# Kernel optimization log

Hardware: AMD Instinct MI355X
Metric: run time of the kernel (lower is better)

Reference implementation:

```python
import jax, jax.numpy as jnp
import numpy as np

N, D, B, C, T, TOD = 8192, 32, 2, 8, 12, 288
PARAM_SCALE = 0.3  # keep relu+softmax logits well-conditioned (original uses plain randn init)


def setup_inputs() -> dict:
    key = jax.random.key(0)
    k0, k1, k2, k3, k4 = jax.random.split(key, 5)
    return {
        "x": jax.random.normal(k0, (B, C, N, T), dtype=jnp.float32),
        "nodevec1": PARAM_SCALE * jax.random.normal(k1, (N, D), dtype=jnp.float32),
        "nodevec2": PARAM_SCALE * jax.random.normal(k2, (N, D), dtype=jnp.float32),
        "timevec": PARAM_SCALE * jax.random.normal(k3, (TOD, D), dtype=jnp.float32),
        "k": PARAM_SCALE * jax.random.normal(k4, (D, D, D), dtype=jnp.float32),
        "time_ind": 100,
    }


def reference(x, nodevec1, nodevec2, timevec, k, time_ind):
    # Dynamic Tucker-decomposition adjacency (SpatialGraphConv.forward, eval mode -> dropout is identity)
    tv = timevec[time_ind]                             # [D]   time_vec
    core = jnp.einsum('d,def->ef', tv, k)              # [D,D] adp1 (squeezed)
    # adp2/adp3 chain: (nodevec1 @ core) @ nodevec2.T  -> [N,N]
    adp = jnp.einsum('ne,ef->nf', nodevec1, core)      # [N,D]
    adp = jnp.einsum('nf,mf->nm', adp, nodevec2)       # [N,N]
    adp = jax.nn.softmax(jax.nn.relu(adp), axis=-1)    # row-softmax over neighbors
    # NConv: neighbor aggregation  'bcnt,nm->bcmt'
    return jnp.einsum('bcnt,nm->bcmt', x, adp)
```

## Files before the change

### kernel.cpp

```cpp
#include <hip/hip_runtime.h>
#include <hip/hip_bf16.h>


#define NN 8192
#define DD 32
#define TT 12
#define NSPLIT 8
#define CHUNK 1024
#define ESTR 70

typedef __attribute__((ext_vector_type(8))) short bf16x8;
typedef __attribute__((ext_vector_type(4))) short bf16x4;
typedef __attribute__((ext_vector_type(4))) float f32x4;

static __device__ __forceinline__ unsigned short f2bf(float f) {
  unsigned int u = __float_as_uint(f);
  u = (u + 0x7FFFu + ((u >> 16) & 1u)) >> 16;
  return (unsigned short)u;
}

static __device__ __forceinline__ float fexp2(float x) {
#if __has_builtin(__builtin_amdgcn_exp2f)
  return __builtin_amdgcn_exp2f(x);
#else
  return __builtin_exp2f(x);
#endif
}

#define RAWBAR()                                          \
  do {                                                    \
    asm volatile("s_waitcnt lgkmcnt(0)" ::: "memory");    \
    __builtin_amdgcn_sched_barrier(0);                    \
    __builtin_amdgcn_s_barrier();                         \
  } while (0)

__global__ __launch_bounds__(256) void k_prep(const float* __restrict__ nv1,
                                              const float* __restrict__ nv2,
                                              const float* __restrict__ timevec,
                                              const float* __restrict__ kk,
                                              const int* __restrict__ tind,
                                              unsigned short* __restrict__ t1b,
                                              unsigned short* __restrict__ nv2b,
                                              float* __restrict__ sums) {
  __shared__ float cs[1024];
  const int tid = threadIdx.x;
  if (tid < 64) sums[blockIdx.x * 64 + tid] = 0.f;
  const float* tv = timevec + (size_t)tind[0] * DD;
  for (int idx = tid; idx < 1024; idx += 256) {
    float acc = 0.f;
#pragma unroll
    for (int d = 0; d < DD; ++d) acc += tv[d] * kk[d * 1024 + idx];
    cs[idx] = acc;
  }
  __syncthreads();
  const int nbase = blockIdx.x * 64;
  const int f = tid & 31, sub = tid >> 5;
#pragma unroll 4
  for (int it = 0; it < 8; ++it) {
    const int n = nbase + it * 8 + sub;
    const float* nr = nv1 + (size_t)n * DD;
    float acc = 0.f;
#pragma unroll
    for (int e = 0; e < DD; ++e) acc += nr[e] * cs[e * DD + f];
    t1b[(size_t)n * DD + f] = f2bf(acc * 1.4426950408889634f);
  }
#pragma unroll 4
  for (int it = 0; it < 8; ++it) {
    const int idx = nbase * DD + it * 256 + tid;
    nv2b[idx] = f2bf(nv2[idx]);
  }
}

__global__ __launch_bounds__(256) void k_stats(const unsigned short* __restrict__ t1b,
                                               const unsigned short* __restrict__ nv2b,
                                               float* __restrict__ sums) {
  const int tid = threadIdx.x;
  const int w = tid >> 6, lane = tid & 63, q = lane >> 4, i16 = lane & 15;
  const int nbase = blockIdx.x * 64 + w * 16;
  bf16x8 a = *(const bf16x8*)(t1b + (size_t)(nbase + i16) * DD + q * 8);
  const f32x4 z4 = {0.f, 0.f, 0.f, 0.f};
  float s[4] = {0.f, 0.f, 0.f, 0.f};
  const int m0 = blockIdx.y * 512;
#define LDB(mt, u) (*(const bf16x8*)(nv2b + (size_t)((mt) + (u)*16 + i16) * DD + q * 8))
  bf16x8 b0 = LDB(m0, 0), b1 = LDB(m0, 1), b2 = LDB(m0, 2), b3 = LDB(m0, 3);
  for (int mt = m0; mt < m0 + 512; mt += 64) {
    const int mtn = (mt + 64 < m0 + 512) ? (mt + 64) : mt;
    bf16x8 n0 = LDB(mtn, 0), n1 = LDB(mtn, 1), n2 = LDB(mtn, 2), n3 = LDB(mtn, 3);
    f32x4 d;
    d = __builtin_amdgcn_mfma_f32_16x16x32_bf16(a, b0, z4, 0, 0, 0);
#pragma unroll
    for (int r = 0; r < 4; ++r) s[r] += fexp2(fmaxf(d[r], 0.f));
    d = __builtin_amdgcn_mfma_f32_16x16x32_bf16(a, b1, z4, 0, 0, 0);
#pragma unroll
    for (int r = 0; r < 4; ++r) s[r] += fexp2(fmaxf(d[r], 0.f));
    d = __builtin_amdgcn_mfma_f32_16x16x32_bf16(a, b2, z4, 0, 0, 0);
#pragma unroll
    for (int r = 0; r < 4; ++r) s[r] += fexp2(fmaxf(d[r], 0.f));
    d = __builtin_amdgcn_mfma_f32_16x16x32_bf16(a, b3, z4, 0, 0, 0);
#pragma unroll
    for (int r = 0; r < 4; ++r) s[r] += fexp2(fmaxf(d[r], 0.f));
    b0 = n0; b1 = n1; b2 = n2; b3 = n3;
  }
#undef LDB
#pragma unroll
  for (int r = 0; r < 4; ++r)
    for (int off = 1; off < 16; off <<= 1) s[r] += __shfl_xor(s[r], off, 64);
  if (i16 == 0) {
#pragma unroll
    for (int r = 0; r < 4; ++r) atomicAdd(&sums[nbase + q * 4 + r], s[r]);
  }
}

__global__ __launch_bounds__(256) void k_y(const float* __restrict__ x,
                                           const float* __restrict__ sums,
                                           unsigned short* __restrict__ yT) {
  __shared__ float xs[3328];
  const int tid = threadIdx.x;
  const int n0 = blockIdx.x * 256;
  const int bc = blockIdx.y;
  const float* xp = x + (size_t)bc * NN * TT + (size_t)n0 * TT;
#pragma unroll
  for (int j = 0; j < 12; ++j) {
    const int idx = j * 256 + tid;
    xs[(idx / 12) * 13 + idx % 12] = xp[idx];
  }
  __syncthreads();
  const float rinv = 1.0f / sums[n0 + tid];
#pragma unroll
  for (int t = 0; t < 12; ++t)
    yT[(size_t)(bc * TT + t) * NN + n0 + tid] = f2bf(xs[tid * 13 + t] * rinv);
}

__global__ __launch_bounds__(256, 4) void k_mega(const unsigned short* __restrict__ t1b,
                                                 const unsigned short* __restrict__ nv2b,
                                                 const unsigned short* __restrict__ yT,
                                                 unsigned short* __restrict__ part) {
  const int tid = threadIdx.x;
  const int w = tid >> 6, lane = tid & 63, q = lane >> 4, i16 = lane & 15;
  const int mb = blockIdx.x * 64;
  const int nt0 = blockIdx.y * CHUNK;

  __shared__ unsigned short Ew[2][64][ESTR];

  const bf16x8 bg = *(const bf16x8*)(nv2b + (size_t)(mb + w * 16 + i16) * DD + q * 8);
  const int rowm = w * 16 + i16;

  const f32x4 z4 = {0.f, 0.f, 0.f, 0.f};
  f32x4 acc[3][4];
#pragma unroll
  for (int c = 0; c < 3; ++c)
#pragma unroll
    for (int ms = 0; ms < 4; ++ms) acc[c][ms] = (f32x4){0.f, 0.f, 0.f, 0.f};

#pragma unroll
  for (int s = 0; s < 4; ++s) {
    bf16x8 at = *(const bf16x8*)(t1b + (size_t)(nt0 + s * 16 + i16) * DD + q * 8);
    f32x4 d = __builtin_amdgcn_mfma_f32_16x16x32_bf16(at, bg, z4, 0, 0, 0);
    bf16x4 e;
#pragma unroll
    for (int r = 0; r < 4; ++r) e[r] = (short)f2bf(fexp2(fmaxf(d[r], 0.f)));
    *(bf16x4*)&Ew[0][rowm][s * 16 + q * 4] = e;
  }
  RAWBAR();

  int p = 0;
  for (int st = 0; st < 16; ++st, p ^= 1) {
    const int nt = nt0 + st * 64;
    const bool more = (st < 15);

    bf16x8 yfr0[3], yfr1[3];
#pragma unroll
    for (int c = 0; c < 3; ++c) {
      const unsigned short* ybase = yT + (size_t)((w * 3 + c) * 16 + i16) * NN + nt + q * 8;
      yfr0[c] = *(const bf16x8*)ybase;
      yfr1[c] = *(const bf16x8*)(ybase + 32);
    }
    bf16x8 atn[4];
    if (more) {
#pragma unroll
      for (int s = 0; s < 4; ++s)
        atn[s] = *(const bf16x8*)(t1b + (size_t)(nt + 64 + s * 16 + i16) * DD + q * 8);
    }

    bf16x8 efr[4];
#pragma unroll
    for (int ms = 0; ms < 4; ++ms)
      efr[ms] = *(const bf16x8*)&Ew[p][ms * 16 + i16][q * 8];

    f32x4 d0, d1;
    if (more) {
      d0 = __builtin_amdgcn_mfma_f32_16x16x32_bf16(atn[0], bg, z4, 0, 0, 0);
      d1 = __builtin_amdgcn_mfma_f32_16x16x32_bf16(atn[1], bg, z4, 0, 0, 0);
    }

    __builtin_amdgcn_s_setprio(1);
#pragma unroll
    for (int c = 0; c < 3; ++c)
#pragma unroll
      for (int ms = 0; ms < 4; ++ms)
        acc[c][ms] = __builtin_amdgcn_mfma_f32_16x16x32_bf16(yfr0[c], efr[ms], acc[c][ms], 0, 0, 0);
    __builtin_amdgcn_s_setprio(0);

    if (more) {
      bf16x4 e0, e1;
#pragma unroll
      for (int r = 0; r < 4; ++r) {
        e0[r] = (short)f2bf(fexp2(fmaxf(d0[r], 0.f)));
        e1[r] = (short)f2bf(fexp2(fmaxf(d1[r], 0.f)));
      }
      *(bf16x4*)&Ew[p ^ 1][rowm][q * 4] = e0;
      *(bf16x4*)&Ew[p ^ 1][rowm][16 + q * 4] = e1;
      f32x4 d2 = __builtin_amdgcn_mfma_f32_16x16x32_bf16(atn[2], bg, z4, 0, 0, 0);
      f32x4 d3 = __builtin_amdgcn_mfma_f32_16x16x32_bf16(atn[3], bg, z4, 0, 0, 0);
      bf16x4 e2, e3;
#pragma unroll
      for (int r = 0; r < 4; ++r) {
        e2[r] = (short)f2bf(fexp2(fmaxf(d2[r], 0.f)));
        e3[r] = (short)f2bf(fexp2(fmaxf(d3[r], 0.f)));
      }
      *(bf16x4*)&Ew[p ^ 1][rowm][32 + q * 4] = e2;
      *(bf16x4*)&Ew[p ^ 1][rowm][48 + q * 4] = e3;
    }

#pragma unroll
    for (int ms = 0; ms < 4; ++ms)
      efr[ms] = *(const bf16x8*)&Ew[p][ms * 16 + i16][32 + q * 8];
    __builtin_amdgcn_s_setprio(1);
#pragma unroll
    for (int c = 0; c < 3; ++c)
#pragma unroll
      for (int ms = 0; ms < 4; ++ms)
        acc[c][ms] = __builtin_amdgcn_mfma_f32_16x16x32_bf16(yfr1[c], efr[ms], acc[c][ms], 0, 0, 0);
    __builtin_amdgcn_s_setprio(0);

    RAWBAR();
  }

  unsigned short* pp = part + (size_t)blockIdx.y * 192 * NN;
#pragma unroll
  for (int c = 0; c < 3; ++c)
#pragma unroll
    for (int ms = 0; ms < 4; ++ms) {
      const int colbase = (w * 3 + c) * 16 + q * 4;
      const int m = mb + ms * 16 + i16;
#pragma unroll
      for (int r = 0; r < 4; ++r)
        pp[(size_t)(colbase + r) * NN + m] = f2bf(acc[c][ms][r]);
    }
}

__global__ __launch_bounds__(256) void k_reduce(const unsigned short* __restrict__ part,
                                                float* __restrict__ out) {
  __shared__ float os[3328];
  const int tid = threadIdx.x;
  const int m0 = blockIdx.x * 256;
  const int bc = blockIdx.y;
#pragma unroll
  for (int t = 0; t < 12; ++t) {
    const int col = bc * TT + t;
    float s = 0.f;
#pragma unroll
    for (int nc = 0; nc < NSPLIT; ++nc) {
      const unsigned int u = part[((size_t)nc * 192 + col) * NN + m0 + tid];
      s += __uint_as_float(u << 16);
    }
    os[tid * 13 + t] = s;
  }
  __syncthreads();
  float* op = out + (size_t)bc * NN * TT + (size_t)m0 * TT;
#pragma unroll
  for (int j = 0; j < 12; ++j) {
    const int idx = j * 256 + tid;
    op[idx] = os[(idx / 12) * 13 + idx % 12];
  }
}

extern "C" void kernel_launch(void* const* d_in, const int* in_sizes, int n_in,
                              void* d_out, int out_size, void* d_ws, size_t ws_size,
                              hipStream_t stream) {
  const float* x = (const float*)d_in[0];
  const float* nv1 = (const float*)d_in[1];
  const float* nv2 = (const float*)d_in[2];
  const float* tv = (const float*)d_in[3];
  const float* kk = (const float*)d_in[4];
  const int* tind = (const int*)d_in[5];
  float* out = (float*)d_out;

  char* ws = (char*)d_ws;
  unsigned short* t1b  = (unsigned short*)(ws);
  unsigned short* nv2b = (unsigned short*)(ws + 524288);
  float* sums          = (float*)(ws + 1048576);
  unsigned short* yT   = (unsigned short*)(ws + 1081344);
  unsigned short* part = (unsigned short*)(ws + 4227072);

  k_prep<<<128, 256, 0, stream>>>(nv1, nv2, tv, kk, tind, t1b, nv2b, sums);
  k_stats<<<dim3(128, 16), 256, 0, stream>>>(t1b, nv2b, sums);
  k_y<<<dim3(32, 16), 256, 0, stream>>>(x, sums, yT);
  k_mega<<<dim3(128, NSPLIT), 256, 0, stream>>>(t1b, nv2b, yT, part);
  k_reduce<<<dim3(32, 16), 256, 0, stream>>>(part, out);
}
```

Baseline: 172.1 us.

## Fold softmax normalization into E tile and merge x transpose into prep kernel

The separate y-scaling kernel is removed. The x transpose to bf16 yT moves into the prep kernel, now launched with 512 blocks. The stats kernel writes per-split partial sums without atomics, which drops the zeroing step. The mega kernel sums the partials into shared memory and multiplies each exp value by the reciprocal row sum before the bf16 conversion. This saves one launch and the atomics, at the cost of every mega block redoing the reciprocal work and extra multiplies inside the hot loop.

Result: slower. 200.7 us (+16.6%).

```diff
diff --git a/kernel.cpp b/kernel.cpp
--- a/kernel.cpp
+++ b/kernel.cpp
@@ -34,17 +34,22 @@
     __builtin_amdgcn_s_barrier();                         \
   } while (0)
 
-__global__ __launch_bounds__(256) void k_prep(const float* __restrict__ nv1,
-                                              const float* __restrict__ nv2,
-                                              const float* __restrict__ timevec,
-                                              const float* __restrict__ kk,
-                                              const int* __restrict__ tind,
-                                              unsigned short* __restrict__ t1b,
-                                              unsigned short* __restrict__ nv2b,
-                                              float* __restrict__ sums) {
+__global__ __launch_bounds__(256) void k_pre(const float* __restrict__ x,
+                                             const float* __restrict__ nv1,
+                                             const float* __restrict__ nv2,
+                                             const float* __restrict__ timevec,
+                                             const float* __restrict__ kk,
+                                             const int* __restrict__ tind,
+                                             unsigned short* __restrict__ t1b,
+                                             unsigned short* __restrict__ nv2b,
+                                             unsigned short* __restrict__ yT) {
   __shared__ float cs[1024];
+  __shared__ float xs[3328];
   const int tid = threadIdx.x;
-  if (tid < 64) sums[blockIdx.x * 64 + tid] = 0.f;
+  const int bid = blockIdx.x;
+  const int bc = bid >> 5, xb = bid & 31;
+  const int n0 = xb * 256;
+
   const float* tv = timevec + (size_t)tind[0] * DD;
   for (int idx = tid; idx < 1024; idx += 256) {
     float acc = 0.f;
@@ -52,39 +57,49 @@
     for (int d = 0; d < DD; ++d) acc += tv[d] * kk[d * 1024 + idx];
     cs[idx] = acc;
   }
+  const float* xp = x + (size_t)bc * NN * TT + (size_t)n0 * TT;
+#pragma unroll
+  for (int j = 0; j < 12; ++j) {
+    const int idx = j * 256 + tid;
+    xs[(idx / 12) * 13 + idx % 12] = xp[idx];
+  }
   __syncthreads();
-  const int nbase = blockIdx.x * 64;
+
   const int f = tid & 31, sub = tid >> 5;
-#pragma unroll 4
-  for (int it = 0; it < 8; ++it) {
-    const int n = nbase + it * 8 + sub;
+  const int tb = bid * 16;
+#pragma unroll
+  for (int it = 0; it < 2; ++it) {
+    const int n = tb + it * 8 + sub;
     const float* nr = nv1 + (size_t)n * DD;
     float acc = 0.f;
 #pragma unroll
     for (int e = 0; e < DD; ++e) acc += nr[e] * cs[e * DD + f];
     t1b[(size_t)n * DD + f] = f2bf(acc * 1.4426950408889634f);
   }
-#pragma unroll 4
-  for (int it = 0; it < 8; ++it) {
-    const int idx = nbase * DD + it * 256 + tid;
+#pragma unroll
+  for (int it = 0; it < 2; ++it) {
+    const int idx = bid * 512 + it * 256 + tid;
     nv2b[idx] = f2bf(nv2[idx]);
   }
+#pragma unroll
+  for (int t = 0; t < 12; ++t)
+    yT[(size_t)(bc * TT + t) * NN + n0 + tid] = f2bf(xs[tid * 13 + t]);
 }
 
 __global__ __launch_bounds__(256) void k_stats(const unsigned short* __restrict__ t1b,
                                                const unsigned short* __restrict__ nv2b,
-                                               float* __restrict__ sums) {
+                                               float* __restrict__ sumsp) {
   const int tid = threadIdx.x;
   const int w = tid >> 6, lane = tid & 63, q = lane >> 4, i16 = lane & 15;
   const int nbase = blockIdx.x * 64 + w * 16;
   bf16x8 a = *(const bf16x8*)(t1b + (size_t)(nbase + i16) * DD + q * 8);
   const f32x4 z4 = {0.f, 0.f, 0.f, 0.f};
   float s[4] = {0.f, 0.f, 0.f, 0.f};
-  const int m0 = blockIdx.y * 512;
+  const int m0 = blockIdx.y * 1024;
 #define LDB(mt, u) (*(const bf16x8*)(nv2b + (size_t)((mt) + (u)*16 + i16) * DD + q * 8))
   bf16x8 b0 = LDB(m0, 0), b1 = LDB(m0, 1), b2 = LDB(m0, 2), b3 = LDB(m0, 3);
-  for (int mt = m0; mt < m0 + 512; mt += 64) {
-    const int mtn = (mt + 64 < m0 + 512) ? (mt + 64) : mt;
+  for (int mt = m0; mt < m0 + 1024; mt += 64) {
+    const int mtn = (mt + 64 < m0 + 1024) ? (mt + 64) : mt;
     bf16x8 n0 = LDB(mtn, 0), n1 = LDB(mtn, 1), n2 = LDB(mtn, 2), n3 = LDB(mtn, 3);
     f32x4 d;
     d = __builtin_amdgcn_mfma_f32_16x16x32_bf16(a, b0, z4, 0, 0, 0);
@@ -107,33 +122,15 @@
     for (int off = 1; off < 16; off <<= 1) s[r] += __shfl_xor(s[r], off, 64);
   if (i16 == 0) {
 #pragma unroll
-    for (int r = 0; r < 4; ++r) atomicAdd(&sums[nbase + q * 4 + r], s[r]);
-  }
-}
-
-__global__ __launch_bounds__(256) void k_y(const float* __restrict__ x,
-                                           const float* __restrict__ sums,
-                                           unsigned short* __restrict__ yT) {
-  __shared__ float xs[3328];
-  const int tid = threadIdx.x;
-  const int n0 = blockIdx.x * 256;
-  const int bc = blockIdx.y;
-  const float* xp = x + (size_t)bc * NN * TT + (size_t)n0 * TT;
-#pragma unroll
-  for (int j = 0; j < 12; ++j) {
-    const int idx = j * 256 + tid;
-    xs[(idx / 12) * 13 + idx % 12] = xp[idx];
-  }
-  __syncthreads();
-  const float rinv = 1.0f / sums[n0 + tid];
-#pragma unroll
-  for (int t = 0; t < 12; ++t)
-    yT[(size_t)(bc * TT + t) * NN + n0 + tid] = f2bf(xs[tid * 13 + t] * rinv);
+    for (int r = 0; r < 4; ++r)
+      sumsp[(size_t)blockIdx.y * NN + nbase + q * 4 + r] = s[r];
+  }
 }
 
 __global__ __launch_bounds__(256, 4) void k_mega(const unsigned short* __restrict__ t1b,
                                                  const unsigned short* __restrict__ nv2b,
                                                  const unsigned short* __restrict__ yT,
+                                                 const float* __restrict__ sumsp,
                                                  unsigned short* __restrict__ part) {
   const int tid = threadIdx.x;
   const int w = tid >> 6, lane = tid & 63, q = lane >> 4, i16 = lane & 15;
@@ -141,6 +138,17 @@
   const int nt0 = blockIdx.y * CHUNK;
 
   __shared__ unsigned short Ew[2][64][ESTR];
+  __shared__ f32x4 rinv_v[256];
+
+  {
+    float* rl = (float*)rinv_v;
+    for (int k = tid; k < 1024; k += 256) {
+      float ssum = 0.f;
+#pragma unroll
+      for (int j = 0; j < NSPLIT; ++j) ssum += sumsp[(size_t)j * NN + nt0 + k];
+      rl[k] = 1.0f / ssum;
+    }
+  }
 
   const bf16x8 bg = *(const bf16x8*)(nv2b + (size_t)(mb + w * 16 + i16) * DD + q * 8);
   const int rowm = w * 16 + i16;
@@ -151,14 +159,17 @@
   for (int c = 0; c < 3; ++c)
 #pragma unroll
     for (int ms = 0; ms < 4; ++ms) acc[c][ms] = (f32x4){0.f, 0.f, 0.f, 0.f};
+
+  RAWBAR();
 
 #pragma unroll
   for (int s = 0; s < 4; ++s) {
     bf16x8 at = *(const bf16x8*)(t1b + (size_t)(nt0 + s * 16 + i16) * DD + q * 8);
     f32x4 d = __builtin_amdgcn_mfma_f32_16x16x32_bf16(at, bg, z4, 0, 0, 0);
+    const f32x4 rv = rinv_v[s * 4 + q];
     bf16x4 e;
 #pragma unroll
-    for (int r = 0; r < 4; ++r) e[r] = (short)f2bf(fexp2(fmaxf(d[r], 0.f)));
+    for (int r = 0; r < 4; ++r) e[r] = (short)f2bf(fexp2(fmaxf(d[r], 0.f)) * rv[r]);
     *(bf16x4*)&Ew[0][rowm][s * 16 + q * 4] = e;
   }
   RAWBAR();
@@ -176,10 +187,13 @@
       yfr1[c] = *(const bf16x8*)(ybase + 32);
     }
     bf16x8 atn[4];
+    f32x4 rv[4];
     if (more) {
 #pragma unroll
-      for (int s = 0; s < 4; ++s)
+      for (int s = 0; s < 4; ++s) {
         atn[s] = *(const bf16x8*)(t1b + (size_t)(nt + 64 + s * 16 + i16) * DD + q * 8);
+        rv[s] = rinv_v[(st + 1) * 16 + s * 4 + q];
+      }
     }
 
     bf16x8 efr[4];
@@ -205,8 +219,8 @@
       bf16x4 e0, e1;
 #pragma unroll
       for (int r = 0; r < 4; ++r) {
-        e0[r] = (short)f2bf(fexp2(fmaxf(d0[r], 0.f)));
-        e1[r] = (short)f2bf(fexp2(fmaxf(d1[r], 0.f)));
+        e0[r] = (short)f2bf(fexp2(fmaxf(d0[r], 0.f)) * rv[0][r]);
+        e1[r] = (short)f2bf(fexp2(fmaxf(d1[r], 0.f)) * rv[1][r]);
       }
       *(bf16x4*)&Ew[p ^ 1][rowm][q * 4] = e0;
       *(bf16x4*)&Ew[p ^ 1][rowm][16 + q * 4] = e1;
@@ -215,8 +229,8 @@
       bf16x4 e2, e3;
 #pragma unroll
       for (int r = 0; r < 4; ++r) {
-        e2[r] = (short)f2bf(fexp2(fmaxf(d2[r], 0.f)));
-        e3[r] = (short)f2bf(fexp2(fmaxf(d3[r], 0.f)));
+        e2[r] = (short)f2bf(fexp2(fmaxf(d2[r], 0.f)) * rv[2][r]);
+        e3[r] = (short)f2bf(fexp2(fmaxf(d3[r], 0.f)) * rv[3][r]);
       }
       *(bf16x4*)&Ew[p ^ 1][rowm][32 + q * 4] = e2;
       *(bf16x4*)&Ew[p ^ 1][rowm][48 + q * 4] = e3;
@@ -289,13 +303,12 @@
   char* ws = (char*)d_ws;
   unsigned short* t1b  = (unsigned short*)(ws);
   unsigned short* nv2b = (unsigned short*)(ws + 524288);
-  float* sums          = (float*)(ws + 1048576);
-  unsigned short* yT   = (unsigned short*)(ws + 1081344);
-  unsigned short* part = (unsigned short*)(ws + 4227072);
-
-  k_prep<<<128, 256, 0, stream>>>(nv1, nv2, tv, kk, tind, t1b, nv2b, sums);
-  k_stats<<<dim3(128, 16), 256, 0, stream>>>(t1b, nv2b, sums);
-  k_y<<<dim3(32, 16), 256, 0, stream>>>(x, sums, yT);
-  k_mega<<<dim3(128, NSPLIT), 256, 0, stream>>>(t1b, nv2b, yT, part);
+  float* sumsp         = (float*)(ws + 1048576);
+  unsigned short* yT   = (unsigned short*)(ws + 1310720);
+  unsigned short* part = (unsigned short*)(ws + 4456448);
+
+  k_pre<<<512, 256, 0, stream>>>(x, nv1, nv2, tv, kk, tind, t1b, nv2b, yT);
+  k_stats<<<dim3(128, NSPLIT), 256, 0, stream>>>(t1b, nv2b, sumsp);
+  k_mega<<<dim3(128, NSPLIT), 256, 0, stream>>>(t1b, nv2b, yT, sumsp, part);
   k_reduce<<<dim3(32, 16), 256, 0, stream>>>(part, out);
 }
```
